# Performance work log

Measured on AMD Instinct MI355X. Metric: run time of the kernel, lower is better.

The kernel has to match this reference:

```python
import jax, jax.numpy as jnp
import numpy as np


def setup_inputs() -> dict:
    key = jax.random.key(0)
    ks = jax.random.split(key, 7)
    B, L, D, N = 4, 4096, 1024, 64
    x = jax.random.normal(ks[0], (B, L, D), dtype=jnp.float32)
    # nn.Linear weights: (out_features, in_features)
    W_in = jax.random.normal(ks[1], (N, D), dtype=jnp.float32) * (1.0 / np.sqrt(D))
    W_out = jax.random.normal(ks[2], (D, N), dtype=jnp.float32) * (1.0 / np.sqrt(N))
    log_A = jax.random.normal(ks[3], (N,), dtype=jnp.float32) * 0.02
    B_param = jax.random.normal(ks[4], (N,), dtype=jnp.float32) * 0.02
    C_param = jax.random.normal(ks[5], (N,), dtype=jnp.float32) * 0.02
    log_dt = jnp.float32(np.log(1.0))  # dt_init = 1.0
    return {"x": x, "W_in": W_in, "W_out": W_out, "log_A": log_A,
            "B_param": B_param, "C_param": C_param, "log_dt": log_dt}


def _zoh_discretize(log_A, B_param, log_dt):
    dt = jnp.exp(log_dt)
    A = -jnp.exp(log_A)
    Abar = jnp.exp(A * dt)
    eps = 1e-06
    small = jnp.abs(A) < eps
    denom = jnp.where(small, jnp.ones_like(A), A)
    frac = (Abar - 1.0) / denom
    frac = jnp.where(small, dt, frac)
    Bbar = frac * B_param
    return Abar, Bbar


def reference(x, W_in, W_out, log_A, B_param, C_param, log_dt):
    # x: (B, L, D)
    Bsz, L, D = x.shape
    N = log_A.shape[0]
    Abar, Bbar = _zoh_discretize(log_A, B_param, log_dt)
    u = jnp.einsum('bld,nd->bln', x, W_in)  # (B, L, N)

    def step(h, u_t):
        h = h * Abar + u_t * Bbar  # (B, N)
        return h, h * C_param

    h0 = jnp.zeros((Bsz, N), dtype=x.dtype)
    _, ys = jax.lax.scan(step, h0, jnp.swapaxes(u, 0, 1))  # ys: (L, B, N)
    y = jnp.swapaxes(ys, 0, 1)  # (B, L, N)
    return jnp.einsum('bln,dn->bld', y, W_out)  # (B, L, D)
```

## Files before the change

kernel.cpp:

```cpp
#include <hip/hip_runtime.h>
#include <math.h>

namespace {

constexpr int kB = 4;
constexpr int kL = 4096;
constexpr int kD = 1024;
constexpr int kN = 64;
constexpr int kM = kB * kL;
constexpr size_t kBLN = (size_t)kM * kN;
constexpr int kSplit = 4;
constexpr int kKRange = kD / kSplit;
constexpr int kChunks = 64;
constexpr int kChunkLen = kL / kChunks;

__global__ __launch_bounds__(64) void k_gemm_in(const float* __restrict__ x,
                                                const float* __restrict__ Win,
                                                float* __restrict__ upart) {
  __shared__ __align__(16) float As[64][68];
  __shared__ __align__(16) float Bs[64][68];
  const int t = threadIdx.x;
  const int m_blk = blockIdx.x * 64;
  const int z = blockIdx.y;

  const int tm = t & 7;
  const int tn = t >> 3;
  const int m0 = tm * 8;
  const int n0 = tn * 8;

  float acc[8][8];
#pragma unroll
  for (int i = 0; i < 8; ++i)
#pragma unroll
    for (int j = 0; j < 8; ++j) acc[i][j] = 0.0f;

  for (int kc = 0; kc < kKRange; kc += 64) {
    const int k0 = z * kKRange + kc;
#pragma unroll
    for (int i = 0; i < 16; ++i) {
      const int m4 = i * 4;
      const float* src = &x[(size_t)(m_blk + m4) * kD + k0 + t];
      float4 v = make_float4(src[0], src[kD], src[2 * kD], src[3 * kD]);
      *reinterpret_cast<float4*>(&As[t][m4]) = v;
    }
#pragma unroll
    for (int i = 0; i < 16; ++i) {
      const int n4 = i * 4;
      const float* src = &Win[(size_t)n4 * kD + k0 + t];
      float4 v = make_float4(src[0], src[kD], src[2 * kD], src[3 * kD]);
      *reinterpret_cast<float4*>(&Bs[t][n4]) = v;
    }
    __syncthreads();

#pragma unroll 4
    for (int k = 0; k < 64; ++k) {
      float4 a0 = *reinterpret_cast<const float4*>(&As[k][m0]);
      float4 a1 = *reinterpret_cast<const float4*>(&As[k][m0 + 4]);
      float4 b0 = *reinterpret_cast<const float4*>(&Bs[k][n0]);
      float4 b1 = *reinterpret_cast<const float4*>(&Bs[k][n0 + 4]);
      float a[8] = {a0.x, a0.y, a0.z, a0.w, a1.x, a1.y, a1.z, a1.w};
      float b[8] = {b0.x, b0.y, b0.z, b0.w, b1.x, b1.y, b1.z, b1.w};
#pragma unroll
      for (int i = 0; i < 8; ++i)
#pragma unroll
        for (int j = 0; j < 8; ++j) acc[i][j] = fmaf(a[i], b[j], acc[i][j]);
    }
    __syncthreads();
  }

  float* up = upart + (size_t)z * kBLN;
#pragma unroll
  for (int i = 0; i < 8; ++i) {
    const size_t o = (size_t)(m_blk + m0 + i) * kN + n0;
    *reinterpret_cast<float4*>(&up[o]) =
        make_float4(acc[i][0], acc[i][1], acc[i][2], acc[i][3]);
    *reinterpret_cast<float4*>(&up[o + 4]) =
        make_float4(acc[i][4], acc[i][5], acc[i][6], acc[i][7]);
  }
}

__device__ __forceinline__ void zoh(const float* __restrict__ logA,
                                    const float* __restrict__ logdt, int n,
                                    float& A, float& dt, float& Abar) {
  dt = expf(logdt[0]);
  A = -expf(logA[n]);
  Abar = expf(A * dt);
}

__device__ __forceinline__ float zoh_bbar(float A, float dt, float Abar,
                                          float Bp) {
  const bool small = fabsf(A) < 1e-6f;
  const float denom = small ? 1.0f : A;
  float frac = (Abar - 1.0f) / denom;
  frac = small ? dt : frac;
  return frac * Bp;
}

__global__ __launch_bounds__(64) void k_scan_local(
    const float* __restrict__ logA, const float* __restrict__ Bparam,
    const float* __restrict__ logdt, float* __restrict__ ws) {
  const int n = threadIdx.x;
  const int c = blockIdx.x;
  const int b = blockIdx.y;
  float A, dt, Abar;
  zoh(logA, logdt, n, A, dt, Abar);
  const float Bbar = zoh_bbar(A, dt, Abar, Bparam[n]);

  float* hloc = ws + 4 * kBLN;
  const size_t base = ((size_t)b * kL + (size_t)c * kChunkLen) * kN + n;

  float h = 0.0f;
#pragma unroll 8
  for (int s = 0; s < kChunkLen; ++s) {
    const size_t idx = base + (size_t)s * kN;
    const float uu = ws[idx] + ws[idx + kBLN] + ws[idx + 2 * kBLN] +
                     ws[idx + 3 * kBLN];
    const float ub = uu * Bbar;
    h = fmaf(h, Abar, ub);
    ws[idx] = ub;
  }
  hloc[((size_t)b * kChunks + c) * kN + n] = h;
}

__global__ __launch_bounds__(64) void k_scan_apply(
    const float* __restrict__ logA, const float* __restrict__ Cparam,
    const float* __restrict__ logdt, float* __restrict__ ws) {
  const int n = threadIdx.x;
  const int c = blockIdx.x;
  const int b = blockIdx.y;
  float A, dt, Abar;
  zoh(logA, logdt, n, A, dt, Abar);
  const float C = Cparam[n];
  const float AbarC = expf(A * dt * (float)kChunkLen);

  const float* hloc = ws + 4 * kBLN;
  const size_t hbase = (size_t)b * kChunks * kN + n;

  float h = 0.0f;
  if (c > 0) {
    float p0 = hloc[hbase];
    float p1 = (c > 1) ? hloc[hbase + kN] : 0.0f;
    for (int j = 0; j < c; ++j) {
      const float cur = p0;
      p0 = p1;
      p1 = (j + 2 < c) ? hloc[hbase + (size_t)(j + 2) * kN] : 0.0f;
      h = fmaf(h, AbarC, cur);
    }
  }

  float* ybuf = ws + kBLN;
  const size_t base = ((size_t)b * kL + (size_t)c * kChunkLen) * kN + n;
#pragma unroll 8
  for (int s = 0; s < kChunkLen; ++s) {
    const size_t idx = base + (size_t)s * kN;
    h = fmaf(h, Abar, ws[idx]);
    ybuf[idx] = h * C;
  }
}

__global__ __launch_bounds__(128) void k_gemm_out(
    const float* __restrict__ y, const float* __restrict__ Wout,
    float* __restrict__ out) {
  __shared__ __align__(16) float Ys[64][68];
  __shared__ __align__(16) float Ws[64][132];
  const int t = threadIdx.x;
  const int m_blk = blockIdx.x * 64;
  const int d_blk = blockIdx.y * 128;

  const int k = t & 63;
  const int w = t >> 6;

#pragma unroll
  for (int i = 0; i < 8; ++i) {
    const int m4 = (i * 2 + w) * 4;
    const float* src = &y[(size_t)(m_blk + m4) * kN + k];
    *reinterpret_cast<float4*>(&Ys[k][m4]) =
        make_float4(src[0], src[kN], src[2 * kN], src[3 * kN]);
  }
#pragma unroll
  for (int i = 0; i < 16; ++i) {
    const int d4 = (i * 2 + w) * 4;
    const float* src = &Wout[(size_t)(d_blk + d4) * kN + k];
    *reinterpret_cast<float4*>(&Ws[k][d4]) =
        make_float4(src[0], src[kN], src[2 * kN], src[3 * kN]);
  }
  __syncthreads();

  const int tm = t & 7;
  const int tn = t >> 3;
  const int m0 = tm * 8;
  const int n0 = tn * 8;

  float acc[8][8];
#pragma unroll
  for (int i = 0; i < 8; ++i)
#pragma unroll
    for (int j = 0; j < 8; ++j) acc[i][j] = 0.0f;

#pragma unroll 4
  for (int kk = 0; kk < 64; ++kk) {
    float4 a0 = *reinterpret_cast<const float4*>(&Ys[kk][m0]);
    float4 a1 = *reinterpret_cast<const float4*>(&Ys[kk][m0 + 4]);
    float4 b0 = *reinterpret_cast<const float4*>(&Ws[kk][n0]);
    float4 b1 = *reinterpret_cast<const float4*>(&Ws[kk][n0 + 4]);
    float a[8] = {a0.x, a0.y, a0.z, a0.w, a1.x, a1.y, a1.z, a1.w};
    float b[8] = {b0.x, b0.y, b0.z, b0.w, b1.x, b1.y, b1.z, b1.w};
#pragma unroll
    for (int i = 0; i < 8; ++i)
#pragma unroll
      for (int j = 0; j < 8; ++j) acc[i][j] = fmaf(a[i], b[j], acc[i][j]);
  }

#pragma unroll
  for (int i = 0; i < 8; ++i) {
    const size_t o = (size_t)(m_blk + m0 + i) * kD + d_blk + n0;
    *reinterpret_cast<float4*>(&out[o]) =
        make_float4(acc[i][0], acc[i][1], acc[i][2], acc[i][3]);
    *reinterpret_cast<float4*>(&out[o + 4]) =
        make_float4(acc[i][4], acc[i][5], acc[i][6], acc[i][7]);
  }
}

}

extern "C" void kernel_launch(void* const* d_in, const int* in_sizes, int n_in,
                              void* d_out, int out_size, void* d_ws,
                              size_t ws_size, hipStream_t stream) {
  const float* x = (const float*)d_in[0];
  const float* Win = (const float*)d_in[1];
  const float* Wout = (const float*)d_in[2];
  const float* logA = (const float*)d_in[3];
  const float* Bparam = (const float*)d_in[4];
  const float* Cparam = (const float*)d_in[5];
  const float* logdt = (const float*)d_in[6];
  float* out = (float*)d_out;
  float* ws = (float*)d_ws;

  k_gemm_in<<<dim3(kM / 64, kSplit), 64, 0, stream>>>(x, Win, ws);
  k_scan_local<<<dim3(kChunks, kB), 64, 0, stream>>>(logA, Bparam, logdt, ws);
  k_scan_apply<<<dim3(kChunks, kB), 64, 0, stream>>>(logA, Cparam, logdt, ws);
  k_gemm_out<<<dim3(kM / 64, kD / 128), 128, 0, stream>>>(ws + kBLN, Wout, out);
}
```

Baseline: 202.9 us.

## Double split-K in input GEMM, shrink K tiles, add atomic fallback path

The input projection now splits K eight ways instead of four and stages 32-wide K tiles, doubling the grid to 2048 blocks to improve occupancy on the skinny GEMM. The output GEMM now loops over 16-wide K tiles instead of loading all of K=64 at once, cutting shared memory per block. A fallback path uses atomicAdd into a zeroed buffer when the workspace is too small for eight partial buffers. The cost is extra partial-sum traffic: the scan kernel reads eight partial buffers instead of four, and smaller K tiles add more barriers.

```diff
diff --git a/kernel.cpp b/kernel.cpp
--- a/kernel.cpp
+++ b/kernel.cpp
@@ -9,16 +9,20 @@
 constexpr int kN = 64;
 constexpr int kM = kB * kL;
 constexpr size_t kBLN = (size_t)kM * kN;
-constexpr int kSplit = 4;
+constexpr int kSplit = 8;
 constexpr int kKRange = kD / kSplit;
+constexpr int kBK1 = 32;
+constexpr int kBK2 = 16;
 constexpr int kChunks = 64;
 constexpr int kChunkLen = kL / kChunks;
-
+constexpr size_t kHloc = (size_t)kB * kChunks * kN;
+
+template <bool kAtomic>
 __global__ __launch_bounds__(64) void k_gemm_in(const float* __restrict__ x,
                                                 const float* __restrict__ Win,
-                                                float* __restrict__ upart) {
-  __shared__ __align__(16) float As[64][68];
-  __shared__ __align__(16) float Bs[64][68];
+                                                float* __restrict__ u) {
+  __shared__ __align__(16) float As[kBK1][68];
+  __shared__ __align__(16) float Bs[kBK1][68];
   const int t = threadIdx.x;
   const int m_blk = blockIdx.x * 64;
   const int z = blockIdx.y;
@@ -28,32 +32,35 @@
   const int m0 = tm * 8;
   const int n0 = tn * 8;
 
+  const int kk = t & 31;
+  const int half = t >> 5;
+
   float acc[8][8];
 #pragma unroll
   for (int i = 0; i < 8; ++i)
 #pragma unroll
     for (int j = 0; j < 8; ++j) acc[i][j] = 0.0f;
 
-  for (int kc = 0; kc < kKRange; kc += 64) {
+  for (int kc = 0; kc < kKRange; kc += kBK1) {
     const int k0 = z * kKRange + kc;
 #pragma unroll
-    for (int i = 0; i < 16; ++i) {
-      const int m4 = i * 4;
-      const float* src = &x[(size_t)(m_blk + m4) * kD + k0 + t];
+    for (int i = 0; i < 8; ++i) {
+      const int m4 = half * 32 + i * 4;
+      const float* src = &x[(size_t)(m_blk + m4) * kD + k0 + kk];
       float4 v = make_float4(src[0], src[kD], src[2 * kD], src[3 * kD]);
-      *reinterpret_cast<float4*>(&As[t][m4]) = v;
-    }
-#pragma unroll
-    for (int i = 0; i < 16; ++i) {
-      const int n4 = i * 4;
-      const float* src = &Win[(size_t)n4 * kD + k0 + t];
+      *reinterpret_cast<float4*>(&As[kk][m4]) = v;
+    }
+#pragma unroll
+    for (int i = 0; i < 8; ++i) {
+      const int n4 = half * 32 + i * 4;
+      const float* src = &Win[(size_t)n4 * kD + k0 + kk];
       float4 v = make_float4(src[0], src[kD], src[2 * kD], src[3 * kD]);
-      *reinterpret_cast<float4*>(&Bs[t][n4]) = v;
+      *reinterpret_cast<float4*>(&Bs[kk][n4]) = v;
     }
     __syncthreads();
 
 #pragma unroll 4
-    for (int k = 0; k < 64; ++k) {
+    for (int k = 0; k < kBK1; ++k) {
       float4 a0 = *reinterpret_cast<const float4*>(&As[k][m0]);
       float4 a1 = *reinterpret_cast<const float4*>(&As[k][m0 + 4]);
       float4 b0 = *reinterpret_cast<const float4*>(&Bs[k][n0]);
@@ -68,14 +75,23 @@
     __syncthreads();
   }
 
-  float* up = upart + (size_t)z * kBLN;
-#pragma unroll
-  for (int i = 0; i < 8; ++i) {
-    const size_t o = (size_t)(m_blk + m0 + i) * kN + n0;
-    *reinterpret_cast<float4*>(&up[o]) =
-        make_float4(acc[i][0], acc[i][1], acc[i][2], acc[i][3]);
-    *reinterpret_cast<float4*>(&up[o + 4]) =
-        make_float4(acc[i][4], acc[i][5], acc[i][6], acc[i][7]);
+  if constexpr (kAtomic) {
+#pragma unroll
+    for (int i = 0; i < 8; ++i) {
+      float* dst = &u[(size_t)(m_blk + m0 + i) * kN + n0];
+#pragma unroll
+      for (int j = 0; j < 8; ++j) atomicAdd(dst + j, acc[i][j]);
+    }
+  } else {
+    float* up = u + (size_t)z * kBLN;
+#pragma unroll
+    for (int i = 0; i < 8; ++i) {
+      const size_t o = (size_t)(m_blk + m0 + i) * kN + n0;
+      *reinterpret_cast<float4*>(&up[o]) =
+          make_float4(acc[i][0], acc[i][1], acc[i][2], acc[i][3]);
+      *reinterpret_cast<float4*>(&up[o + 4]) =
+          make_float4(acc[i][4], acc[i][5], acc[i][6], acc[i][7]);
+    }
   }
 }
 
@@ -96,9 +112,11 @@
   return frac * Bp;
 }
 
+template <int kParts>
 __global__ __launch_bounds__(64) void k_scan_local(
     const float* __restrict__ logA, const float* __restrict__ Bparam,
-    const float* __restrict__ logdt, float* __restrict__ ws) {
+    const float* __restrict__ logdt, float* __restrict__ u,
+    float* __restrict__ hloc) {
   const int n = threadIdx.x;
   const int c = blockIdx.x;
   const int b = blockIdx.y;
@@ -106,25 +124,26 @@
   zoh(logA, logdt, n, A, dt, Abar);
   const float Bbar = zoh_bbar(A, dt, Abar, Bparam[n]);
 
-  float* hloc = ws + 4 * kBLN;
   const size_t base = ((size_t)b * kL + (size_t)c * kChunkLen) * kN + n;
 
   float h = 0.0f;
 #pragma unroll 8
   for (int s = 0; s < kChunkLen; ++s) {
     const size_t idx = base + (size_t)s * kN;
-    const float uu = ws[idx] + ws[idx + kBLN] + ws[idx + 2 * kBLN] +
-                     ws[idx + 3 * kBLN];
+    float uu = 0.0f;
+#pragma unroll
+    for (int p = 0; p < kParts; ++p) uu += u[idx + (size_t)p * kBLN];
     const float ub = uu * Bbar;
     h = fmaf(h, Abar, ub);
-    ws[idx] = ub;
+    u[idx] = ub;
   }
   hloc[((size_t)b * kChunks + c) * kN + n] = h;
 }
 
 __global__ __launch_bounds__(64) void k_scan_apply(
     const float* __restrict__ logA, const float* __restrict__ Cparam,
-    const float* __restrict__ logdt, float* __restrict__ ws) {
+    const float* __restrict__ logdt, const float* __restrict__ u,
+    float* __restrict__ ybuf, const float* __restrict__ hloc) {
   const int n = threadIdx.x;
   const int c = blockIdx.x;
   const int b = blockIdx.y;
@@ -133,7 +152,6 @@
   const float C = Cparam[n];
   const float AbarC = expf(A * dt * (float)kChunkLen);
 
-  const float* hloc = ws + 4 * kBLN;
   const size_t hbase = (size_t)b * kChunks * kN + n;
 
   float h = 0.0f;
@@ -148,12 +166,11 @@
     }
   }
 
-  float* ybuf = ws + kBLN;
   const size_t base = ((size_t)b * kL + (size_t)c * kChunkLen) * kN + n;
 #pragma unroll 8
   for (int s = 0; s < kChunkLen; ++s) {
     const size_t idx = base + (size_t)s * kN;
-    h = fmaf(h, Abar, ws[idx]);
+    h = fmaf(h, Abar, u[idx]);
     ybuf[idx] = h * C;
   }
 }
@@ -161,30 +178,14 @@
 __global__ __launch_bounds__(128) void k_gemm_out(
     const float* __restrict__ y, const float* __restrict__ Wout,
     float* __restrict__ out) {
-  __shared__ __align__(16) float Ys[64][68];
-  __shared__ __align__(16) float Ws[64][132];
+  __shared__ __align__(16) float Ys[kBK2][68];
+  __shared__ __align__(16) float Ws[kBK2][132];
   const int t = threadIdx.x;
   const int m_blk = blockIdx.x * 64;
   const int d_blk = blockIdx.y * 128;
 
-  const int k = t & 63;
-  const int w = t >> 6;
-
-#pragma unroll
-  for (int i = 0; i < 8; ++i) {
-    const int m4 = (i * 2 + w) * 4;
-    const float* src = &y[(size_t)(m_blk + m4) * kN + k];
-    *reinterpret_cast<float4*>(&Ys[k][m4]) =
-        make_float4(src[0], src[kN], src[2 * kN], src[3 * kN]);
-  }
-#pragma unroll
-  for (int i = 0; i < 16; ++i) {
-    const int d4 = (i * 2 + w) * 4;
-    const float* src = &Wout[(size_t)(d_blk + d4) * kN + k];
-    *reinterpret_cast<float4*>(&Ws[k][d4]) =
-        make_float4(src[0], src[kN], src[2 * kN], src[3 * kN]);
-  }
-  __syncthreads();
+  const int kk = t & 15;
+  const int g = t >> 4;
 
   const int tm = t & 7;
   const int tn = t >> 3;
@@ -197,18 +198,37 @@
 #pragma unroll
     for (int j = 0; j < 8; ++j) acc[i][j] = 0.0f;
 
+  for (int kc = 0; kc < kN; kc += kBK2) {
+#pragma unroll
+    for (int i = 0; i < 2; ++i) {
+      const int m4 = g * 8 + i * 4;
+      const float* src = &y[(size_t)(m_blk + m4) * kN + kc + kk];
+      *reinterpret_cast<float4*>(&Ys[kk][m4]) =
+          make_float4(src[0], src[kN], src[2 * kN], src[3 * kN]);
+    }
+#pragma unroll
+    for (int i = 0; i < 4; ++i) {
+      const int d4 = g * 16 + i * 4;
+      const float* src = &Wout[(size_t)(d_blk + d4) * kN + kc + kk];
+      *reinterpret_cast<float4*>(&Ws[kk][d4]) =
+          make_float4(src[0], src[kN], src[2 * kN], src[3 * kN]);
+    }
+    __syncthreads();
+
 #pragma unroll 4
-  for (int kk = 0; kk < 64; ++kk) {
-    float4 a0 = *reinterpret_cast<const float4*>(&Ys[kk][m0]);
-    float4 a1 = *reinterpret_cast<const float4*>(&Ys[kk][m0 + 4]);
-    float4 b0 = *reinterpret_cast<const float4*>(&Ws[kk][n0]);
-    float4 b1 = *reinterpret_cast<const float4*>(&Ws[kk][n0 + 4]);
-    float a[8] = {a0.x, a0.y, a0.z, a0.w, a1.x, a1.y, a1.z, a1.w};
-    float b[8] = {b0.x, b0.y, b0.z, b0.w, b1.x, b1.y, b1.z, b1.w};
-#pragma unroll
-    for (int i = 0; i < 8; ++i)
-#pragma unroll
-      for (int j = 0; j < 8; ++j) acc[i][j] = fmaf(a[i], b[j], acc[i][j]);
+    for (int k = 0; k < kBK2; ++k) {
+      float4 a0 = *reinterpret_cast<const float4*>(&Ys[k][m0]);
+      float4 a1 = *reinterpret_cast<const float4*>(&Ys[k][m0 + 4]);
+      float4 b0 = *reinterpret_cast<const float4*>(&Ws[k][n0]);
+      float4 b1 = *reinterpret_cast<const float4*>(&Ws[k][n0 + 4]);
+      float a[8] = {a0.x, a0.y, a0.z, a0.w, a1.x, a1.y, a1.z, a1.w};
+      float b[8] = {b0.x, b0.y, b0.z, b0.w, b1.x, b1.y, b1.z, b1.w};
+#pragma unroll
+      for (int i = 0; i < 8; ++i)
+#pragma unroll
+        for (int j = 0; j < 8; ++j) acc[i][j] = fmaf(a[i], b[j], acc[i][j]);
+    }
+    __syncthreads();
   }
 
 #pragma unroll
@@ -236,8 +256,26 @@
   float* out = (float*)d_out;
   float* ws = (float*)d_ws;
 
-  k_gemm_in<<<dim3(kM / 64, kSplit), 64, 0, stream>>>(x, Win, ws);
-  k_scan_local<<<dim3(kChunks, kB), 64, 0, stream>>>(logA, Bparam, logdt, ws);
-  k_scan_apply<<<dim3(kChunks, kB), 64, 0, stream>>>(logA, Cparam, logdt, ws);
-  k_gemm_out<<<dim3(kM / 64, kD / 128), 128, 0, stream>>>(ws + kBLN, Wout, out);
-}
+  const bool partials = ws_size >= (8 * kBLN + kHloc) * sizeof(float);
+
+  if (partials) {
+    float* hloc = ws + 8 * kBLN;
+    k_gemm_in<false><<<dim3(kM / 64, kSplit), 64, 0, stream>>>(x, Win, ws);
+    k_scan_local<kSplit><<<dim3(kChunks, kB), 64, 0, stream>>>(
+        logA, Bparam, logdt, ws, hloc);
+    k_scan_apply<<<dim3(kChunks, kB), 64, 0, stream>>>(
+        logA, Cparam, logdt, ws, ws + kBLN, hloc);
+    k_gemm_out<<<dim3(kM / 64, kD / 128), 128, 0, stream>>>(ws + kBLN, Wout,
+                                                            out);
+  } else {
+    float* hloc = ws + 2 * kBLN;
+    hipMemsetAsync(ws, 0, kBLN * sizeof(float), stream);
+    k_gemm_in<true><<<dim3(kM / 64, kSplit), 64, 0, stream>>>(x, Win, ws);
+    k_scan_local<1><<<dim3(kChunks, kB), 64, 0, stream>>>(logA, Bparam, logdt,
+                                                          ws, hloc);
+    k_scan_apply<<<dim3(kChunks, kB), 64, 0, stream>>>(
+        logA, Cparam, logdt, ws, ws + kBLN, hloc);
+    k_gemm_out<<<dim3(kM / 64, kD / 128), 128, 0, stream>>>(ws + kBLN, Wout,
+                                                            out);
+  }
+}
```

Measured after the change: 206.6 us. Within noise of the previous version (+1.8%).
